# Kernel tuning notes

Measured on AMD Instinct MI355X. Metric: run time of the kernel, lower is better.

The kernel has to match this reference:

```python
import jax, jax.numpy as jnp
import numpy as np

M, N, C, D = 2, 8, 1024, 256  # n_routers, num_adapters, channel_dim, down_sample_size
B, S = 32, 512


def setup_inputs() -> dict:
    key = jax.random.key(0)
    k1, k2, k3, k4, k5 = jax.random.split(key, 5)
    x = jax.random.normal(k1, (B, S, C), dtype=jnp.float32)
    expert_index = jax.random.randint(k2, (M, B), 0, N, dtype=jnp.int32)
    down_w = jax.random.normal(k3, (M, N, C, D), dtype=jnp.float32) * 0.01
    down_b = jax.random.normal(k4, (M, N, D), dtype=jnp.float32) * 0.01
    up_w = jax.random.normal(k5, (M, N, D, C), dtype=jnp.float32) * 0.01
    return {"x": x, "expert_index": expert_index, "down_w": down_w,
            "down_b": down_b, "up_w": up_w}


def reference(x, expert_index, down_w, down_b, up_w):
    # Gather per-(router, batch-element) adapter weights along the adapter axis.
    idx = expert_index  # [M, B]
    bw_down = jnp.take_along_axis(down_w, idx[:, :, None, None], axis=1)  # [M, B, C, D]
    bb_down = jnp.take_along_axis(down_b, idx[:, :, None], axis=1)        # [M, B, D]
    bw_up = jnp.take_along_axis(up_w, idx[:, :, None, None], axis=1)      # [M, B, D, C]
    # z = swish(x @ W_down + b_down)  -> [M, B, S, D]
    z = jnp.einsum('bsc,mbcd->mbsd', x, bw_down) + bb_down[:, :, None, :]
    z = jax.nn.silu(z)
    # u = z @ W_up -> [M, B, S, C]
    u = jnp.einsum('mbsd,mbdc->mbsc', z, bw_up)
    return u
```

## Files before the change

kernel.cpp:

```cpp
#include <hip/hip_runtime.h>
#include <stdint.h>

typedef unsigned short u16;
typedef __bf16 bf16x8 __attribute__((ext_vector_type(8)));
typedef float f32x4 __attribute__((ext_vector_type(4)));

#define MM 2
#define NN 8
#define CC 1024
#define DD 256
#define BB 32
#define SS 512

__device__ __forceinline__ u16 f2bf(float f) {
  uint32_t u = __float_as_uint(f);
  u += 0x7FFFu + ((u >> 16) & 1u);
  return (u16)(u >> 16);
}

__device__ __forceinline__ void async16(const void* g, void* l) {
  __builtin_amdgcn_global_load_lds(
      (const __attribute__((address_space(1))) uint32_t*)g,
      (__attribute__((address_space(3))) uint32_t*)l, 16, 0, 0);
}

#define CVT_BLOCKS 16384
#define T_BLOCKS 4096
__global__ __launch_bounds__(256) void prep(
    const float* __restrict__ x, u16* __restrict__ xb,
    const float* __restrict__ dw, u16* __restrict__ wdT,
    const float* __restrict__ uw, u16* __restrict__ wuT) {
  const int bid = blockIdx.x;
  if (bid < CVT_BLOCKS) {
    int i = (bid * 256 + threadIdx.x) * 4;
    float4 v = *reinterpret_cast<const float4*>(x + i);
    u16 o[4] = {f2bf(v.x), f2bf(v.y), f2bf(v.z), f2bf(v.w)};
    *reinterpret_cast<uint2*>(xb + i) = *reinterpret_cast<const uint2*>(o);
    return;
  }
  __shared__ float tile[32][33];
  const float* src;
  u16* dst;
  int R, L, bx, by, slab;
  if (bid < CVT_BLOCKS + T_BLOCKS) {
    int t = bid - CVT_BLOCKS;
    slab = t >> 8;
    int t2 = t & 255;
    bx = t2 & 7;  by = t2 >> 3;
    R = CC; L = DD;
    src = dw; dst = wdT;
  } else {
    int t = bid - CVT_BLOCKS - T_BLOCKS;
    slab = t >> 8;
    int t2 = t & 255;
    bx = t2 & 31; by = t2 >> 5;
    R = DD; L = CC;
    src = uw; dst = wuT;
  }
  src += (size_t)slab * R * L;
  dst += (size_t)slab * R * L;
  const int c0 = bx * 32, r0 = by * 32;
  const int tx = threadIdx.x & 31, ty = threadIdx.x >> 5;
#pragma unroll
  for (int i = 0; i < 32; i += 8)
    tile[ty + i][tx] = src[(size_t)(r0 + ty + i) * L + c0 + tx];
  __syncthreads();
#pragma unroll
  for (int i = 0; i < 32; i += 8)
    dst[(size_t)(c0 + ty + i) * R + r0 + tx] = f2bf(tile[tx][ty + i]);
}

__global__ __launch_bounds__(256) void fused_adapter(
    const u16* __restrict__ xb, const u16* __restrict__ wdT,
    const u16* __restrict__ wuT, const float* __restrict__ db,
    const int* __restrict__ eidx, float* __restrict__ out) {
  __shared__ __align__(16) u16 smA[64 * 32];
  __shared__ __align__(16) u16 smB[256 * 32];
  __shared__ __align__(16) u16 zl[8 * 64 * 32];

  const int pair = blockIdx.y;
  const int m = pair >> 5;
  const int b = pair & 31;
  const int e = eidx[pair];
  const int s0 = blockIdx.x * 64;

  const int tid = threadIdx.x;
  const int lane = tid & 63;
  const int wave = tid >> 6;
  const int quad = lane >> 4;
  const int l16 = lane & 15;

  const int srow = lane >> 2;
  const int kc = (lane & 3) * 8;

  const u16* Ab = xb + ((size_t)b * SS + s0) * CC;
  const u16* Bd = wdT + (size_t)(m * NN + e) * DD * CC;
  const u16* gA = Ab + (size_t)(wave * 16 + srow) * CC + kc;
  u16* lA = smA + wave * 16 * 32;
  const u16* gB[4];
  u16* lB[4];
#pragma unroll
  for (int t = 0; t < 4; ++t) {
    gB[t] = Bd + (size_t)(t * 64 + wave * 16 + srow) * CC + kc;
    lB[t] = smB + (t * 64 + wave * 16) * 32;
  }

  f32x4 acc[4][4];
#pragma unroll
  for (int i = 0; i < 4; ++i)
#pragma unroll
    for (int j = 0; j < 4; ++j) acc[i][j] = (f32x4){0.f, 0.f, 0.f, 0.f};

  for (int kk = 0; kk < CC; kk += 32) {
    async16(gA + kk, lA);
#pragma unroll
    for (int t = 0; t < 4; ++t) async16(gB[t] + kk, lB[t]);
    __syncthreads();
    bf16x8 af[4], bfr[4];
#pragma unroll
    for (int i = 0; i < 4; ++i)
      af[i] = *reinterpret_cast<const bf16x8*>(&smA[(i * 16 + l16) * 32 + quad * 8]);
#pragma unroll
    for (int j = 0; j < 4; ++j)
      bfr[j] = *reinterpret_cast<const bf16x8*>(&smB[(wave * 64 + j * 16 + l16) * 32 + quad * 8]);
#pragma unroll
    for (int i = 0; i < 4; ++i)
#pragma unroll
      for (int j = 0; j < 4; ++j)
        acc[i][j] = __builtin_amdgcn_mfma_f32_16x16x32_bf16(af[i], bfr[j], acc[i][j], 0, 0, 0);
    __syncthreads();
  }

  const float* bias_p = db + (size_t)(m * NN + e) * DD;
#pragma unroll
  for (int j = 0; j < 4; ++j) {
    const int d = wave * 64 + j * 16 + l16;
    const float bias = bias_p[d];
    const int kt = d >> 5;
    const int kl = d & 31;
#pragma unroll
    for (int i = 0; i < 4; ++i) {
      const int sr = i * 16 + quad * 4;
#pragma unroll
      for (int r = 0; r < 4; ++r) {
        float v = acc[i][j][r] + bias;
        v = v / (1.f + __expf(-v));
        zl[(kt * 64 + sr + r) * 32 + kl] = f2bf(v);
      }
    }
  }
  __syncthreads();

  const u16* Bu = wuT + (size_t)(m * NN + e) * CC * DD;
  float* ob = out + ((size_t)pair * SS + s0) * CC;

  for (int ct = 0; ct < 4; ++ct) {
    const u16* gB2[4];
#pragma unroll
    for (int t = 0; t < 4; ++t)
      gB2[t] = Bu + (size_t)(ct * 256 + t * 64 + wave * 16 + srow) * DD + kc;

#pragma unroll
    for (int i = 0; i < 4; ++i)
#pragma unroll
      for (int j = 0; j < 4; ++j) acc[i][j] = (f32x4){0.f, 0.f, 0.f, 0.f};

    for (int kk = 0; kk < DD; kk += 32) {
#pragma unroll
      for (int t = 0; t < 4; ++t) async16(gB2[t] + kk, lB[t]);
      __syncthreads();
      bf16x8 af[4], bfr[4];
      const int it = kk >> 5;
#pragma unroll
      for (int i = 0; i < 4; ++i)
        af[i] = *reinterpret_cast<const bf16x8*>(&zl[(it * 64 + i * 16 + l16) * 32 + quad * 8]);
#pragma unroll
      for (int j = 0; j < 4; ++j)
        bfr[j] = *reinterpret_cast<const bf16x8*>(&smB[(wave * 64 + j * 16 + l16) * 32 + quad * 8]);
#pragma unroll
      for (int i = 0; i < 4; ++i)
#pragma unroll
        for (int j = 0; j < 4; ++j)
          acc[i][j] = __builtin_amdgcn_mfma_f32_16x16x32_bf16(af[i], bfr[j], acc[i][j], 0, 0, 0);
      __syncthreads();
    }

#pragma unroll
    for (int j = 0; j < 4; ++j) {
      const int c = ct * 256 + wave * 64 + j * 16 + l16;
#pragma unroll
      for (int i = 0; i < 4; ++i) {
        const int sr = i * 16 + quad * 4;
#pragma unroll
        for (int r = 0; r < 4; ++r)
          ob[(size_t)(sr + r) * CC + c] = acc[i][j][r];
      }
    }
  }
}

extern "C" void kernel_launch(void* const* d_in, const int* in_sizes, int n_in,
                              void* d_out, int out_size, void* d_ws, size_t ws_size,
                              hipStream_t stream) {
  const float* x  = (const float*)d_in[0];
  const int* eidx = (const int*)d_in[1];
  const float* dw = (const float*)d_in[2];
  const float* db = (const float*)d_in[3];
  const float* uw = (const float*)d_in[4];
  float* out = (float*)d_out;

  char* ws = (char*)d_ws;
  u16* xb  = (u16*)(ws);
  u16* wdT = (u16*)(ws + (size_t)32 * 1024 * 1024);
  u16* wuT = (u16*)(ws + (size_t)40 * 1024 * 1024);

  prep<<<dim3(CVT_BLOCKS + 2 * T_BLOCKS), dim3(256), 0, stream>>>(
      x, xb, dw, wdT, uw, wuT);
  fused_adapter<<<dim3(SS / 64, MM * BB), dim3(256), 0, stream>>>(
      xb, wdT, wuT, db, eidx, out);
}
```

Before: 275.6 us.

## Double-buffer LDS loads and enlarge tile to 128 rows with 8 waves

The fused adapter kernel now uses 512 threads and processes 128 sequence rows per block, laid out as a 2x4 wave grid. This halves how often each weight tile is reloaded per row. Global-to-LDS loads are double-buffered so the next k-slice is fetched while MFMAs run on the current one, which drops one barrier per iteration. The up-projection loop is flattened across column tiles, and its first weight slice is prefetched during the last down-projection step. LDS use grows to about 112 KB and the grid shrinks to half as many blocks, which may limit occupancy.

```diff
diff --git a/kernel.cpp b/kernel.cpp
--- a/kernel.cpp
+++ b/kernel.cpp
@@ -70,19 +70,19 @@
     dst[(size_t)(c0 + ty + i) * R + r0 + tx] = f2bf(tile[tx][ty + i]);
 }
 
-__global__ __launch_bounds__(256) void fused_adapter(
+__global__ __launch_bounds__(512, 2) void fused_adapter(
     const u16* __restrict__ xb, const u16* __restrict__ wdT,
     const u16* __restrict__ wuT, const float* __restrict__ db,
     const int* __restrict__ eidx, float* __restrict__ out) {
-  __shared__ __align__(16) u16 smA[64 * 32];
-  __shared__ __align__(16) u16 smB[256 * 32];
-  __shared__ __align__(16) u16 zl[8 * 64 * 32];
+  __shared__ __align__(16) u16 smA[2][128 * 32];
+  __shared__ __align__(16) u16 smB[2][256 * 32];
+  __shared__ __align__(16) u16 zl[8 * 128 * 32];
 
   const int pair = blockIdx.y;
   const int m = pair >> 5;
   const int b = pair & 31;
   const int e = eidx[pair];
-  const int s0 = blockIdx.x * 64;
+  const int s0 = blockIdx.x * 128;
 
   const int tid = threadIdx.x;
   const int lane = tid & 63;
@@ -93,17 +93,19 @@
   const int srow = lane >> 2;
   const int kc = (lane & 3) * 8;
 
+  const int wr = (wave >> 2) * 64;
+  const int wc = (wave & 3) * 64;
+
   const u16* Ab = xb + ((size_t)b * SS + s0) * CC;
   const u16* Bd = wdT + (size_t)(m * NN + e) * DD * CC;
+  const u16* Bu = wuT + (size_t)(m * NN + e) * CC * DD;
+
   const u16* gA = Ab + (size_t)(wave * 16 + srow) * CC + kc;
-  u16* lA = smA + wave * 16 * 32;
-  const u16* gB[4];
-  u16* lB[4];
-#pragma unroll
-  for (int t = 0; t < 4; ++t) {
-    gB[t] = Bd + (size_t)(t * 64 + wave * 16 + srow) * CC + kc;
-    lB[t] = smB + (t * 64 + wave * 16) * 32;
-  }
+  const u16* gB0 = Bd + (size_t)(wave * 32 + srow) * CC + kc;
+  const u16* gB1 = Bd + (size_t)(wave * 32 + 16 + srow) * CC + kc;
+  const int lAo = wave * 16 * 32;
+  const int lB0o = (wave * 32) * 32;
+  const int lB1o = (wave * 32 + 16) * 32;
 
   f32x4 acc[4][4];
 #pragma unroll
@@ -111,18 +113,29 @@
 #pragma unroll
     for (int j = 0; j < 4; ++j) acc[i][j] = (f32x4){0.f, 0.f, 0.f, 0.f};
 
-  for (int kk = 0; kk < CC; kk += 32) {
-    async16(gA + kk, lA);
-#pragma unroll
-    for (int t = 0; t < 4; ++t) async16(gB[t] + kk, lB[t]);
-    __syncthreads();
+  async16(gA, &smA[0][lAo]);
+  async16(gB0, &smB[0][lB0o]);
+  async16(gB1, &smB[0][lB1o]);
+  __syncthreads();
+
+  for (int kk = 0; kk < 32; ++kk) {
+    const int cur = kk & 1, nxt = cur ^ 1;
+    if (kk < 31) {
+      const int ko = (kk + 1) * 32;
+      async16(gA + ko, &smA[nxt][lAo]);
+      async16(gB0 + ko, &smB[nxt][lB0o]);
+      async16(gB1 + ko, &smB[nxt][lB1o]);
+    } else {
+      async16(Bu + (size_t)(wave * 32 + srow) * DD + kc, &smB[nxt][lB0o]);
+      async16(Bu + (size_t)(wave * 32 + 16 + srow) * DD + kc, &smB[nxt][lB1o]);
+    }
     bf16x8 af[4], bfr[4];
 #pragma unroll
     for (int i = 0; i < 4; ++i)
-      af[i] = *reinterpret_cast<const bf16x8*>(&smA[(i * 16 + l16) * 32 + quad * 8]);
+      af[i] = *reinterpret_cast<const bf16x8*>(&smA[cur][(wr + i * 16 + l16) * 32 + quad * 8]);
 #pragma unroll
     for (int j = 0; j < 4; ++j)
-      bfr[j] = *reinterpret_cast<const bf16x8*>(&smB[(wave * 64 + j * 16 + l16) * 32 + quad * 8]);
+      bfr[j] = *reinterpret_cast<const bf16x8*>(&smB[cur][(wc + j * 16 + l16) * 32 + quad * 8]);
 #pragma unroll
     for (int i = 0; i < 4; ++i)
 #pragma unroll
@@ -134,68 +147,68 @@
   const float* bias_p = db + (size_t)(m * NN + e) * DD;
 #pragma unroll
   for (int j = 0; j < 4; ++j) {
-    const int d = wave * 64 + j * 16 + l16;
+    const int d = wc + j * 16 + l16;
     const float bias = bias_p[d];
     const int kt = d >> 5;
     const int kl = d & 31;
 #pragma unroll
     for (int i = 0; i < 4; ++i) {
-      const int sr = i * 16 + quad * 4;
+      const int zr = wr + i * 16 + quad * 4;
 #pragma unroll
       for (int r = 0; r < 4; ++r) {
         float v = acc[i][j][r] + bias;
         v = v / (1.f + __expf(-v));
-        zl[(kt * 64 + sr + r) * 32 + kl] = f2bf(v);
+        zl[(kt * 128 + zr + r) * 32 + kl] = f2bf(v);
       }
     }
   }
   __syncthreads();
 
-  const u16* Bu = wuT + (size_t)(m * NN + e) * CC * DD;
   float* ob = out + ((size_t)pair * SS + s0) * CC;
 
-  for (int ct = 0; ct < 4; ++ct) {
-    const u16* gB2[4];
-#pragma unroll
-    for (int t = 0; t < 4; ++t)
-      gB2[t] = Bu + (size_t)(ct * 256 + t * 64 + wave * 16 + srow) * DD + kc;
-
-#pragma unroll
-    for (int i = 0; i < 4; ++i)
-#pragma unroll
-      for (int j = 0; j < 4; ++j) acc[i][j] = (f32x4){0.f, 0.f, 0.f, 0.f};
-
-    for (int kk = 0; kk < DD; kk += 32) {
-#pragma unroll
-      for (int t = 0; t < 4; ++t) async16(gB2[t] + kk, lB[t]);
-      __syncthreads();
-      bf16x8 af[4], bfr[4];
-      const int it = kk >> 5;
+  for (int g = 0; g < 32; ++g) {
+    const int cur = g & 1, nxt = cur ^ 1;
+    const int ct = g >> 3;
+    const int it = g & 7;
+    if (g < 31) {
+      const int g2 = g + 1;
+      const int ct2 = g2 >> 3;
+      const int ko2 = (g2 & 7) * 32;
+      async16(Bu + (size_t)(ct2 * 256 + wave * 32 + srow) * DD + ko2 + kc, &smB[nxt][lB0o]);
+      async16(Bu + (size_t)(ct2 * 256 + wave * 32 + 16 + srow) * DD + ko2 + kc, &smB[nxt][lB1o]);
+    }
+    if (it == 0) {
 #pragma unroll
       for (int i = 0; i < 4; ++i)
-        af[i] = *reinterpret_cast<const bf16x8*>(&zl[(it * 64 + i * 16 + l16) * 32 + quad * 8]);
+#pragma unroll
+        for (int j = 0; j < 4; ++j) acc[i][j] = (f32x4){0.f, 0.f, 0.f, 0.f};
+    }
+    bf16x8 af[4], bfr[4];
+#pragma unroll
+    for (int i = 0; i < 4; ++i)
+      af[i] = *reinterpret_cast<const bf16x8*>(&zl[(it * 128 + wr + i * 16 + l16) * 32 + quad * 8]);
+#pragma unroll
+    for (int j = 0; j < 4; ++j)
+      bfr[j] = *reinterpret_cast<const bf16x8*>(&smB[cur][(wc + j * 16 + l16) * 32 + quad * 8]);
+#pragma unroll
+    for (int i = 0; i < 4; ++i)
 #pragma unroll
       for (int j = 0; j < 4; ++j)
-        bfr[j] = *reinterpret_cast<const bf16x8*>(&smB[(wave * 64 + j * 16 + l16) * 32 + quad * 8]);
-#pragma unroll
-      for (int i = 0; i < 4; ++i)
-#pragma unroll
-        for (int j = 0; j < 4; ++j)
-          acc[i][j] = __builtin_amdgcn_mfma_f32_16x16x32_bf16(af[i], bfr[j], acc[i][j], 0, 0, 0);
-      __syncthreads();
-    }
-
-#pragma unroll
-    for (int j = 0; j < 4; ++j) {
-      const int c = ct * 256 + wave * 64 + j * 16 + l16;
-#pragma unroll
-      for (int i = 0; i < 4; ++i) {
-        const int sr = i * 16 + quad * 4;
-#pragma unroll
-        for (int r = 0; r < 4; ++r)
-          ob[(size_t)(sr + r) * CC + c] = acc[i][j][r];
+        acc[i][j] = __builtin_amdgcn_mfma_f32_16x16x32_bf16(af[i], bfr[j], acc[i][j], 0, 0, 0);
+    if (it == 7) {
+#pragma unroll
+      for (int j = 0; j < 4; ++j) {
+        const int c = ct * 256 + wc + j * 16 + l16;
+#pragma unroll
+        for (int i = 0; i < 4; ++i) {
+          const int sr = wr + i * 16 + quad * 4;
+#pragma unroll
+          for (int r = 0; r < 4; ++r)
+            ob[(size_t)(sr + r) * CC + c] = acc[i][j][r];
+        }
       }
     }
+    __syncthreads();
   }
 }
 
@@ -216,6 +229,6 @@
 
   prep<<<dim3(CVT_BLOCKS + 2 * T_BLOCKS), dim3(256), 0, stream>>>(
       x, xb, dw, wdT, uw, wuT);
-  fused_adapter<<<dim3(SS / 64, MM * BB), dim3(256), 0, stream>>>(
+  fused_adapter<<<dim3(SS / 128, MM * BB), dim3(512), 0, stream>>>(
       xb, wdT, wuT, db, eidx, out);
 }
```

Measured after the change: 277.5 us. No clear change (+0.7%).
